# Optimization experiments

Hardware: AMD Instinct MI355X
Metric: run time of the kernel (lower is better)

The kernel has to match this reference:

```python
import jax, jax.numpy as jnp
import numpy as np

B, EMBED, H, W = 2, 32, 96, 96
SQ = (4, 2); R = 2; EXP = 2
SCH = EMBED // SQ[0]            # 8  squeezed channel dim
SHSP = SCH * R * R              # 32 shuffled spatial dim
SSP = SHSP // SQ[1]             # 16 squeezed spatial dim (attention embed dim)
HEADS = SCH * EXP               # 16
EACH = SSP // SCH               # 2
IDX = np.array([i + j * SCH for i in range(SCH) for j in range(EACH)])
NIDX = np.array([i + j * EACH for i in range(EACH) for j in range(SCH)])


def conv(x, w, b, stride=1, pad=0, groups=1):
    y = jax.lax.conv_general_dilated(x, w, (stride, stride), [(pad, pad), (pad, pad)],
                                     feature_group_count=groups,
                                     dimension_numbers=('NCHW', 'OIHW', 'NCHW'))
    return y + b[None, :, None, None]


def ln_ch(x, w, b):
    # LayerNorm over channel dim (torch applies it on [B,HW,C])
    mu = x.mean(1, keepdims=True)
    var = ((x - mu) ** 2).mean(1, keepdims=True)
    return (x - mu) * jax.lax.rsqrt(var + 1e-5) * w[None, :, None, None] + b[None, :, None, None]


def l2n(x, axis):
    # F.normalize: divide by L2 norm clamped to eps
    return x / jnp.maximum(jnp.sqrt(jnp.sum(x * x, axis=axis, keepdims=True)), 1e-12)


def _qkv(x, wqkv, bqkv):
    Bb, C, Hh, Ww = x.shape
    qkv = conv(x, wqkv, bqkv, groups=C)                        # [B, C*EXP*3, H, W], per-channel 1x1
    qkv = qkv.reshape(Bb, C, EXP * 3, Hh, Ww).transpose(0, 2, 1, 3, 4)
    q, k, v = jnp.split(qkv, 3, axis=1)                        # each [B, EXP, C, H, W]
    hd = EXP * C // HEADS
    rs = lambda a: a.reshape(Bb, HEADS, hd, Hh * Ww)
    return rs(q), rs(k), rs(v)


def _fuse(o, wfus, bfus, Bb, C, Hh, Ww):
    o = o.reshape(Bb, EXP, C, Hh, Ww).transpose(0, 2, 1, 3, 4).reshape(Bb, C * EXP, Hh, Ww)
    return conv(o, wfus, bfus, groups=C)


def chan_attn(x, wqkv, bqkv, t, wfus, bfus):
    Bb, C, Hh, Ww = x.shape
    q, k, v = _qkv(x, wqkv, bqkv)
    q, k = l2n(q, -1), l2n(k, -1)
    a = jax.nn.softmax(jnp.einsum('bhdn,bhen->bhde', q, k) * t, axis=-1)   # [B,h,d,d]
    o = jnp.einsum('bhde,bhen->bhdn', a, v)
    return _fuse(o, wfus, bfus, Bb, C, Hh, Ww)


def spat_attn(x, wqkv, bqkv, t, wfus, bfus):
    Bb, C, Hh, Ww = x.shape
    q, k, v = _qkv(x, wqkv, bqkv)
    q, k = l2n(q, -2), l2n(k, -2)
    a = jax.nn.softmax(jnp.einsum('bhdn,bhdm->bhnm', q, k) * t, axis=-1)   # [B,h,HW,HW]
    o = jnp.einsum('bhnm,bhdm->bhdn', a, v)
    return _fuse(o, wfus, bfus, Bb, C, Hh, Ww)


def pixel_shuffle(x, r):
    Bb, C, Hh, Ww = x.shape
    x = x.reshape(Bb, C // (r * r), r, r, Hh, Ww).transpose(0, 1, 4, 2, 5, 3)
    return x.reshape(Bb, C // (r * r), Hh * r, Ww * r)


def _forward(x, ln1_w, ln1_b, cab_w1, cab_b1, cab_w2, cab_b2, cab_aw1, cab_ab1, cab_aw2, cab_ab2,
             sq1_w, sq1_b, sq2_w, sq2_b, ca_qkv_w, ca_qkv_b, ca_t, ca_fus_w, ca_fus_b,
             sa_qkv_w, sa_qkv_b, sa_t, sa_fus_w, sa_fus_b, un1_w, un1_b, un2_w, un2_b,
             ln2_w, ln2_b, da_w1, da_b1, da_dw_w, da_dw_b, da_pw, da_pb):
    Bb, C, Hh, Ww = x.shape
    xn = ln_ch(x, ln1_w, ln1_b)
    # ---- CAB branch (conv-GELU-conv + RCAN channel attention) ----
    c = jax.nn.gelu(conv(xn, cab_w1, cab_b1, pad=1), approximate=False)
    c = conv(c, cab_w2, cab_b2, pad=1)
    y = c.mean((2, 3), keepdims=True)
    y = jax.nn.relu(conv(y, cab_aw1, cab_ab1))
    y = jax.nn.sigmoid(conv(y, cab_aw2, cab_ab2))
    x_cab = c * y
    # ---- Condensed attention branch ----
    z = conv(xn, sq1_w, sq1_b)                                   # 1x1: C -> SCH
    z = conv(z, sq2_w, sq2_b, stride=R, groups=SCH)              # grouped RxR stride R: -> [B,SSP,H/R,W/R]
    z = z[:, IDX]
    z = chan_attn(z, ca_qkv_w, ca_qkv_b, ca_t, ca_fus_w, ca_fus_b)
    z = z[:, NIDX]
    z = spat_attn(z, sa_qkv_w, sa_qkv_b, sa_t, sa_fus_w, sa_fus_b)
    z = conv(z, un1_w, un1_b, groups=SCH)                        # SSP -> SHSP
    z = pixel_shuffle(z, R)                                      # -> [B,SCH,H,W]
    z = conv(z, un2_w, un2_b)                                    # SCH -> C
    x = x + z + x_cab
    # ---- Dual adaptive (gated depthwise-conv FFN) ----
    xn2 = ln_ch(x, ln2_w, ln2_b)
    d = conv(xn2, da_w1, da_b1)
    d = conv(d, da_dw_w, da_dw_b, pad=3, groups=C).reshape(Bb, C, 2, Hh, Ww)
    d = jax.nn.gelu(d[:, :, 0], approximate=False) * jax.nn.sigmoid(d[:, :, 1])
    d = conv(d, da_pw, da_pb)
    return x + d


def setup_inputs():
    key = jax.random.key(0)
    ks = iter(jax.random.split(key, 40))
    nrm = lambda s: jax.random.normal(next(ks), s, jnp.float32) * 0.05
    inp = {'x': jax.random.normal(next(ks), (B, EMBED, H, W), jnp.float32)}
    wshapes = {
        'cab_w1': (EMBED // 4, EMBED, 3, 3), 'cab_w2': (EMBED, EMBED // 4, 3, 3),
        'cab_aw1': (EMBED // 18, EMBED, 1, 1), 'cab_aw2': (EMBED, EMBED // 18, 1, 1),
        'sq1_w': (SCH, EMBED, 1, 1), 'sq2_w': (SSP, 1, R, R),
        'ca_qkv_w': (SSP * EXP * 3, 1, 1, 1), 'ca_fus_w': (SSP, EXP, 1, 1),
        'sa_qkv_w': (SSP * EXP * 3, 1, 1, 1), 'sa_fus_w': (SSP, EXP, 1, 1),
        'un1_w': (SHSP, SSP // SCH, 1, 1), 'un2_w': (EMBED, SCH, 1, 1),
        'da_w1': (EMBED, EMBED, 1, 1), 'da_dw_w': (2 * EMBED, 1, 7, 7), 'da_pw': (EMBED, EMBED, 1, 1),
    }
    bshapes = {'cab_b1': EMBED // 4, 'cab_b2': EMBED, 'cab_ab1': EMBED // 18, 'cab_ab2': EMBED,
               'sq1_b': SCH, 'sq2_b': SSP, 'ca_qkv_b': SSP * EXP * 3, 'ca_fus_b': SSP,
               'sa_qkv_b': SSP * EXP * 3, 'sa_fus_b': SSP, 'un1_b': SHSP, 'un2_b': EMBED,
               'da_b1': EMBED, 'da_dw_b': 2 * EMBED, 'da_pb': EMBED}
    for n, s in wshapes.items():
        inp[n] = nrm(s)
    for n, s in bshapes.items():
        inp[n] = nrm((s,))
    inp['ln1_w'] = jnp.ones((EMBED,), jnp.float32); inp['ln1_b'] = jnp.zeros((EMBED,), jnp.float32)
    inp['ln2_w'] = jnp.ones((EMBED,), jnp.float32); inp['ln2_b'] = jnp.zeros((EMBED,), jnp.float32)
    inp['ca_t'] = jnp.ones((1, HEADS, 1, 1), jnp.float32)
    inp['sa_t'] = jnp.ones((1, HEADS, 1, 1), jnp.float32)
    return inp


def reference(x, ln1_w, ln1_b, cab_w1, cab_b1, cab_w2, cab_b2, cab_aw1, cab_ab1, cab_aw2, cab_ab2,
              sq1_w, sq1_b, sq2_w, sq2_b, ca_qkv_w, ca_qkv_b, ca_t, ca_fus_w, ca_fus_b,
              sa_qkv_w, sa_qkv_b, sa_t, sa_fus_w, sa_fus_b, un1_w, un1_b, un2_w, un2_b,
              ln2_w, ln2_b, da_w1, da_b1, da_dw_w, da_dw_b, da_pw, da_pb):
    return _forward(x, ln1_w, ln1_b, cab_w1, cab_b1, cab_w2, cab_b2, cab_aw1, cab_ab1, cab_aw2, cab_ab2,
                    sq1_w, sq1_b, sq2_w, sq2_b, ca_qkv_w, ca_qkv_b, ca_t, ca_fus_w, ca_fus_b,
                    sa_qkv_w, sa_qkv_b, sa_t, sa_fus_w, sa_fus_b, un1_w, un1_b, un2_w, un2_b,
                    ln2_w, ln2_b, da_w1, da_b1, da_dw_w, da_dw_b, da_pw, da_pb)
```

## Files before the change

kernel.cpp:

```cpp
#include <hip/hip_runtime.h>
#include <cstdint>
#include <math.h>

#define NP 9216
#define NP2 2304
#define KH 12
#define NMOM 78

__device__ __forceinline__ float gelu_ex(float v){
  return 0.5f*v*(1.0f+erff(v*0.70710678118654752440f));
}
__device__ __forceinline__ float sigm(float v){
  return 1.0f/(1.0f+__expf(-v));
}

__global__ __launch_bounds__(256) void k_ln1(const float* __restrict__ x,
    const float* __restrict__ lw, const float* __restrict__ lb,
    const float* __restrict__ sw, const float* __restrict__ sb,
    float* __restrict__ xn, float* __restrict__ z1)
{
  __shared__ float sred[2][8][32];
  __shared__ float xnsh[32][33];
  int p = threadIdx.x & 31, sl = threadIdx.x >> 5;
  int pix = blockIdx.x*32 + p;
  int b = pix / NP, n = pix % NP;
  const float* xp = x + (size_t)b*32*NP + (size_t)(sl*4)*NP + n;
  float v[4]; float s=0.f, s2=0.f;
#pragma unroll
  for (int c=0;c<4;c++){ float t=xp[(size_t)c*NP]; v[c]=t; s+=t; s2+=t*t; }
  sred[0][sl][p]=s; sred[1][sl][p]=s2;
  __syncthreads();
  s=0.f; s2=0.f;
#pragma unroll
  for (int g=0;g<8;g++){ s += sred[0][g][p]; s2 += sred[1][g][p]; }
  float mu = s*(1.f/32.f);
  float var = s2*(1.f/32.f)-mu*mu;
  float rs = rsqrtf(var+1e-5f);
  float* xo = xn + (size_t)b*32*NP + (size_t)(sl*4)*NP + n;
#pragma unroll
  for (int c=0;c<4;c++){
    int cc = sl*4+c;
    float t = (v[c]-mu)*rs*lw[cc]+lb[cc];
    xo[(size_t)c*NP] = t;
    xnsh[p][cc] = t;
  }
  __syncthreads();
  float vv[32];
#pragma unroll
  for (int c=0;c<32;c++) vv[c]=xnsh[p][c];
  int g = sl;
  float a = sb[g];
#pragma unroll
  for (int c=0;c<32;c++) a += vv[c]*sw[g*32+c];
  z1[(size_t)b*8*NP + (size_t)g*NP + n] = a;
}

__global__ __launch_bounds__(256) void k_phB(const float* __restrict__ xn,
    const float* __restrict__ w1, const float* __restrict__ b1,
    const float* __restrict__ z1, const float* __restrict__ w2,
    const float* __restrict__ b2,
    float* __restrict__ c1, float* __restrict__ u, float* __restrict__ spart)
{
  if (blockIdx.x < 576){
    int og = blockIdx.x/72, pb = blockIdx.x%72;
    int idx = pb*256+threadIdx.x;
    int b = idx/NP, n = idx%NP, i = n/96, j = n%96;
    float acc = b1[og];
    const float* xb = xn + (size_t)b*32*NP;
    const float* wb = w1 + og*288;
#pragma unroll
    for (int di=0;di<3;di++){
      int ii=i+di-1; if ((unsigned)ii>=96u) continue;
#pragma unroll
      for (int dj=0;dj<3;dj++){
        int jj=j+dj-1; if ((unsigned)jj>=96u) continue;
        const float* xp = xb + ii*96+jj;
        const float* wp = wb + di*3+dj;
#pragma unroll
        for (int c=0;c<32;c++) acc += xp[(size_t)c*NP]*wp[c*9];
      }
    }
    c1[(size_t)b*8*NP + (size_t)og*NP + n] = gelu_ex(acc);
  } else {
    __shared__ float red[4][5];
    int u2 = blockIdx.x-576;
    int pr = u2/18, pb = u2%18;
    int idx = pb*256+threadIdx.x;
    int b = idx/NP2, n = idx%NP2, i = n/48, j = n%48;
    int ocA = pr, ocB = pr+8;
    int gA = ocA>>1, gB = ocB>>1;
    const float* zpA = z1 + ((size_t)b*8+gA)*NP + (size_t)(2*i)*96 + 2*j;
    const float* zpB = z1 + ((size_t)b*8+gB)*NP + (size_t)(2*i)*96 + 2*j;
    float vA = zpA[0]*w2[ocA*4]+zpA[1]*w2[ocA*4+1]+zpA[96]*w2[ocA*4+2]+zpA[97]*w2[ocA*4+3]+b2[ocA];
    float vB = zpB[0]*w2[ocB*4]+zpB[1]*w2[ocB*4+1]+zpB[96]*w2[ocB*4+2]+zpB[97]*w2[ocB*4+3]+b2[ocB];
    u[((size_t)b*16+2*pr)*NP2 + n]   = vA;
    u[((size_t)b*16+2*pr+1)*NP2 + n] = vB;
    int wv=threadIdx.x>>6, ln=threadIdx.x&63;
    float st[5]={vA,vB,vA*vA,vB*vB,vA*vB};
#pragma unroll
    for (int k=0;k<5;k++){
      float r=st[k];
#pragma unroll
      for (int m=1;m<64;m<<=1) r+=__shfl_xor(r,m,64);
      if (ln==0) red[wv][k]=r;
    }
    __syncthreads();
    if (threadIdx.x<5){
      float r = red[0][threadIdx.x]+red[1][threadIdx.x]+red[2][threadIdx.x]+red[3][threadIdx.x];
      spart[(b*9 + (pb%9))*40 + pr*5 + threadIdx.x] = r;
    }
  }
}

__global__ __launch_bounds__(256) void k_phC(const float* __restrict__ c1,
    const float* __restrict__ w2, const float* __restrict__ b2,
    float* __restrict__ cbuf, float* __restrict__ ypart,
    const float* __restrict__ u, const float* __restrict__ spart,
    const float* __restrict__ cqw, const float* __restrict__ cqb,
    const float* __restrict__ cat, const float* __restrict__ cfw,
    const float* __restrict__ cfb,
    const float* __restrict__ qw, const float* __restrict__ qb,
    float2* __restrict__ qarr, float* __restrict__ mompart)
{
  if (blockIdx.x < 576){
    __shared__ float red[4][4];
    int og = blockIdx.x/72, pb = blockIdx.x%72;
    int idx = pb*256+threadIdx.x;
    int b = idx/NP, n = idx%NP, i = n/96, j = n%96;
    float acc[4];
#pragma unroll
    for (int k=0;k<4;k++) acc[k]=b2[og*4+k];
    const float* cb = c1 + (size_t)b*8*NP;
#pragma unroll
    for (int di=0;di<3;di++){
      int ii=i+di-1; if ((unsigned)ii>=96u) continue;
#pragma unroll
      for (int dj=0;dj<3;dj++){
        int jj=j+dj-1; if ((unsigned)jj>=96u) continue;
        const float* xp = cb + ii*96+jj;
#pragma unroll
        for (int c=0;c<8;c++){
          float val = xp[(size_t)c*NP];
          const float* wp = w2 + (og*4)*72 + c*9+di*3+dj;
#pragma unroll
          for (int k=0;k<4;k++) acc[k] += val*wp[k*72];
        }
      }
    }
    int wv = threadIdx.x>>6, ln = threadIdx.x&63;
#pragma unroll
    for (int k=0;k<4;k++){
      cbuf[(size_t)b*32*NP + (size_t)(og*4+k)*NP + n] = acc[k];
      float r = acc[k];
#pragma unroll
      for (int m=1;m<64;m<<=1) r += __shfl_xor(r, m, 64);
      if (ln==0) red[wv][k]=r;
    }
    __syncthreads();
    if (threadIdx.x<4){
      float r = red[0][threadIdx.x]+red[1][threadIdx.x]+red[2][threadIdx.x]+red[3][threadIdx.x];
      ypart[(og*72+pb)*4 + threadIdx.x] = r;
    }
  } else {
    __shared__ float red16[16][80];
    int u2 = blockIdx.x-576;
    int bh = u2/9, ch = u2%9;
    int n = ch*256 + threadIdx.x;
    int b = bh>>4, h = bh&15;
    int p = h&7, s = h>>3;
    int cc0=2*p, cc1=2*p+1;
    int oc0 = 2*(cc0&7)+(cc0>>3);
    int oc1 = 2*(cc1&7)+(cc1>>3);
    float AA[2], BB[2], CCc[2];
#pragma unroll
    for (int t2=0;t2<2;t2++){
      int oc = t2? oc1:oc0;
      int p2 = oc>>1, dd = oc&1;
      float st[5]={0,0,0,0,0};
      for (int ib=0; ib<9; ib++){
#pragma unroll
        for (int k=0;k<5;k++) st[k] += spart[(b*9+ib)*40 + p2*5 + k];
      }
      float S0=st[0],S1=st[1],Q00=st[2],Q11=st[3],Q01=st[4];
      float Sd = dd? S1:S0;
      float Qdd = dd? Q11:Q00;
      float cu0[2],cu1[2],ccst[2];
#pragma unroll
      for (int hh=0;hh<2;hh++){
        int h2=p2+8*hh;
        float th2=cat[h2];
        float aq=cqw[(2*p2+dd)*6+hh], bq=cqb[(2*p2+dd)*6+hh];
        float nq=fmaxf(sqrtf(fmaxf(aq*aq*Qdd+2.f*aq*bq*Sd+2304.f*bq*bq,0.f)),1e-12f);
        float m2[2],av[2],bv[2];
#pragma unroll
        for (int e=0;e<2;e++){
          float Se_=e?S1:S0, Qee=e?Q11:Q00, Qde=(dd==e)?Qdd:Q01;
          float ak=cqw[(2*p2+e)*6+2+hh], bk=cqb[(2*p2+e)*6+2+hh];
          float nk=fmaxf(sqrtf(fmaxf(ak*ak*Qee+2.f*ak*bk*Se_+2304.f*bk*bk,0.f)),1e-12f);
          float D=aq*ak*Qde + aq*bk*Sd + bq*ak*Se_ + 2304.f*bq*bk;
          m2[e]=th2*D/(nq*nk);
          av[e]=cqw[(2*p2+e)*6+4+hh]; bv[e]=cqb[(2*p2+e)*6+4+hh];
        }
        float mx=fmaxf(m2[0],m2[1]);
        float e0=__expf(m2[0]-mx), e1=__expf(m2[1]-mx);
        float inv=1.f/(e0+e1);
        cu0[hh]=e0*inv*av[0]; cu1[hh]=e1*inv*av[1]; ccst[hh]=e0*inv*bv[0]+e1*inv*bv[1];
      }
      float f0=cfw[oc*2], f1=cfw[oc*2+1];
      AA[t2]=f0*cu0[0]+f1*cu0[1];
      BB[t2]=f0*cu1[0]+f1*cu1[1];
      CCc[t2]=f0*ccst[0]+f1*ccst[1]+cfb[oc];
    }
    const float* u00 = u + ((size_t)b*16 + (oc0>>1)*2)*NP2;
    const float* u01 = u00 + NP2;
    const float* u10 = u + ((size_t)b*16 + (oc1>>1)*2)*NP2;
    const float* u11 = u10 + NP2;
    float w0 = AA[0]*u00[n]+BB[0]*u01[n]+CCc[0];
    float w1 = AA[1]*u10[n]+BB[1]*u11[n]+CCc[1];
    float k0 = qw[cc0*6+2+s]*w0+qb[cc0*6+2+s];
    float k1 = qw[cc1*6+2+s]*w1+qb[cc1*6+2+s];
    float rnk = 1.f/fmaxf(sqrtf(k0*k0+k1*k1),1e-12f);
    float kc = k0*rnk, ks = k1*rnk;
    float q0 = qw[cc0*6+s]*w0+qb[cc0*6+s];
    float q1 = qw[cc1*6+s]*w1+qb[cc1*6+s];
    float rnq = 1.f/fmaxf(sqrtf(q0*q0+q1*q1),1e-12f);
    qarr[bh*NP2+n] = make_float2(q0*rnq, q1*rnq);

    int grp = threadIdx.x>>4, gl = threadIdx.x&15;
    float c = 1.f, sn = 0.f;
#pragma unroll
    for (int k=0;k<=KH;k++){
      float vals[6] = {c, sn, c*w0, sn*w0, c*w1, sn*w1};
#pragma unroll
      for (int jv=0;jv<6;jv++){
        float r = vals[jv];
        r += __shfl_xor(r, 1, 64);
        r += __shfl_xor(r, 2, 64);
        r += __shfl_xor(r, 4, 64);
        r += __shfl_xor(r, 8, 64);
        if (gl==0) red16[grp][k*6+jv] = r;
      }
      float cn = c*kc - sn*ks;
      sn = sn*kc + c*ks;
      c = cn;
    }
    __syncthreads();
    if (threadIdx.x < NMOM){
      float r = 0.f;
#pragma unroll
      for (int g=0;g<16;g++) r += red16[g][threadIdx.x];
      mompart[(bh*9+ch)*NMOM + threadIdx.x] = r;
    }
  }
}

__global__ __launch_bounds__(256) void k_rows(const float2* __restrict__ qarr,
    const float* __restrict__ mompart, const float* __restrict__ sat,
    const float* __restrict__ qw, const float* __restrict__ qb,
    const float* __restrict__ fw, const float* __restrict__ fb,
    const float* __restrict__ u1w, const float* __restrict__ u1b,
    float* __restrict__ ps)
{
  int bp = blockIdx.x/9, ch = blockIdx.x%9;
  int b = bp>>3, p = bp&7;
  int n = ch*256 + (int)threadIdx.x;
  __shared__ float msh[2][80];
  __shared__ float fsh[2][13];
  int tid = threadIdx.x;
  if (tid < 26){
    int hh = tid/13, k = tid%13;
    double t = (double)sat[p+8*hh];
    double fac;
    if (fabs(t) < 1e-3){
      double xh = 0.5*t;
      double pk = 1.0;
      for (int q=1;q<=k;q++) pk *= xh/(double)q;
      double Ik = pk*(1.0 + xh*xh/(double)(k+1));
      fac = (k? 2.0:1.0)*Ik;
    } else {
      const int KS = 36;
      double ip1 = 0.0, ik = 1e-280, sum2 = 0.0;
      double vk = 0.0, v0 = 0.0;
      for (int q=KS; q>=1; --q){
        if (q == k) vk = ik;
        sum2 += ik;
        double im1 = ip1 + (2.0*(double)q/t)*ik;
        ip1 = ik; ik = im1;
      }
      v0 = ik;
      if (k == 0) vk = v0;
      double total = v0 + 2.0*sum2;
      double scale = exp(t)/total;
      fac = (k? 2.0:1.0)*vk*scale;
    }
    fsh[hh][k] = (float)fac;
  }
  if (tid < 2*NMOM){
    int hh = tid/NMOM, jj = tid%NMOM;
    float ssum = 0.f;
    for (int ib=0; ib<9; ib++)
      ssum += mompart[((size_t)(b*16+p+8*hh)*9+ib)*NMOM + jj];
    msh[hh][jj] = ssum;
  }
  __syncthreads();
  if (tid < 2*NMOM){
    int hh = tid/NMOM, jj = tid%NMOM;
    msh[hh][jj] *= fsh[hh][jj/6];
  }
  __syncthreads();
  float o[2][2];
#pragma unroll
  for (int hh=0;hh<2;hh++){
    float2 q = qarr[(size_t)(b*16+p+8*hh)*NP2 + n];
    float c = 1.f, sn = 0.f;
    float Se=0.f, S0=0.f, S1=0.f;
#pragma unroll
    for (int k=0;k<=KH;k++){
      const float* mk = &msh[hh][k*6];
      Se += c*mk[0] + sn*mk[1];
      S0 += c*mk[2] + sn*mk[3];
      S1 += c*mk[4] + sn*mk[5];
      float cn = c*q.x - sn*q.y;
      sn = sn*q.x + c*q.y;
      c = cn;
    }
    float rSe = 1.f/Se;
    float av0=qw[(2*p)*6+4+hh],  bv0=qb[(2*p)*6+4+hh];
    float av1=qw[(2*p+1)*6+4+hh],bv1=qb[(2*p+1)*6+4+hh];
    o[hh][0]=av0*S0*rSe+bv0;
    o[hh][1]=av1*S1*rSe+bv1;
  }
  float zz0 = o[0][0]*fw[(2*p)*2]   + o[1][0]*fw[(2*p)*2+1]   + fb[2*p];
  float zz1 = o[0][1]*fw[(2*p+1)*2] + o[1][1]*fw[(2*p+1)*2+1] + fb[2*p+1];
  int i=n/48, j=n%48;
  float* pb2 = ps + ((size_t)b*8+p)*NP;
#pragma unroll
  for (int k=0;k<4;k++){
    int od = 4*p+k;
    float v = zz0*u1w[od*2] + zz1*u1w[od*2+1] + u1b[od];
    pb2[(size_t)(2*i+(k>>1))*96 + 2*j + (k&1)] = v;
  }
}

__global__ __launch_bounds__(256) void k_un2(const float* __restrict__ ps,
    const float* __restrict__ ypart,
    const float* __restrict__ aw1, const float* __restrict__ ab1,
    const float* __restrict__ aw2, const float* __restrict__ ab2,
    const float* __restrict__ u2w, const float* __restrict__ u2b,
    const float* __restrict__ x, const float* __restrict__ cbuf,
    const float* __restrict__ lw, const float* __restrict__ lb,
    const float* __restrict__ dw1, const float* __restrict__ db1,
    float* __restrict__ xsum, float* __restrict__ d1)
{
  __shared__ float sred[2][8][32];
  __shared__ float xsh[32][33];
  __shared__ float y2sh[32];
  int p = threadIdx.x & 31, sl = threadIdx.x >> 5;
  int pix = blockIdx.x*32 + p;
  int b = pix/NP, n = pix%NP;
  if (threadIdx.x < 32){
    int c = threadIdx.x;
    float ssum = 0.f;
    for (int ib=0; ib<36; ib++)
      ssum += ypart[((c>>2)*72 + b*36 + ib)*4 + (c&3)];
    float pr = ssum*(1.f/9216.f)*aw1[c];
#pragma unroll
    for (int m=1;m<32;m<<=1) pr += __shfl_xor(pr, m, 64);
    float y1 = fmaxf(pr+ab1[0], 0.f);
    y2sh[c] = sigm(aw2[c]*y1+ab2[c]);
  }
  float pg[8];
#pragma unroll
  for (int g=0;g<8;g++) pg[g]=ps[((size_t)b*8+g)*NP+n];
  __syncthreads();
  float xv[4]; float s=0.f,s2=0.f;
#pragma unroll
  for (int c=0;c<4;c++){
    int cc = sl*4+c;
    float a=u2b[cc];
#pragma unroll
    for (int g=0;g<8;g++) a+=pg[g]*u2w[cc*8+g];
    size_t off=((size_t)b*32+cc)*NP+n;
    float t = x[off]+a+cbuf[off]*y2sh[cc];
    xv[c]=t; xsum[off]=t; s+=t; s2+=t*t;
  }
  sred[0][sl][p]=s; sred[1][sl][p]=s2;
  __syncthreads();
  s=0.f; s2=0.f;
#pragma unroll
  for (int g=0;g<8;g++){ s += sred[0][g][p]; s2 += sred[1][g][p]; }
  float mu=s*(1.f/32.f), var=s2*(1.f/32.f)-mu*mu, rs=rsqrtf(var+1e-5f);
#pragma unroll
  for (int c=0;c<4;c++){
    int cc = sl*4+c;
    xsh[p][cc] = (xv[c]-mu)*rs*lw[cc]+lb[cc];
  }
  __syncthreads();
  float vv[32];
#pragma unroll
  for (int c=0;c<32;c++) vv[c]=xsh[p][c];
#pragma unroll
  for (int k=0;k<4;k++){
    int o = sl*4+k;
    float a=db1[o];
#pragma unroll
    for (int cc=0;cc<32;cc++) a+=vv[cc]*dw1[o*32+cc];
    d1[((size_t)b*32+o)*NP+n]=a;
  }
}

__global__ __launch_bounds__(256) void k_dw(const float* __restrict__ d1,
    const float* __restrict__ w, const float* __restrict__ bias,
    float* __restrict__ dg)
{
  int idx = blockIdx.x*256+threadIdx.x;
  int pl = idx/4608, n2 = idx%4608;
  int i2 = n2/96, j = n2%96;
  int c = pl&31;
  const float* dp = d1 + (size_t)pl*NP;
  const float* w0p = w + (2*c)*49;
  const float* w1p = w + (2*c+1)*49;
  float a0=bias[2*c], a1=bias[2*c+1];
  float c0=bias[2*c], c1=bias[2*c+1];
#pragma unroll
  for (int di=0;di<8;di++){
    int ii=2*i2-3+di; if ((unsigned)ii>=96u) continue;
    const float* rowp = dp + ii*96;
    float t[7];
#pragma unroll
    for (int dj=0;dj<7;dj++){
      int jj=j+dj-3;
      t[dj] = ((unsigned)jj<96u) ? rowp[jj] : 0.f;
    }
    if (di<7){
#pragma unroll
      for (int dj=0;dj<7;dj++){ a0 += t[dj]*w0p[di*7+dj]; a1 += t[dj]*w1p[di*7+dj]; }
    }
    if (di>0){
#pragma unroll
      for (int dj=0;dj<7;dj++){ c0 += t[dj]*w0p[(di-1)*7+dj]; c1 += t[dj]*w1p[(di-1)*7+dj]; }
    }
  }
  dg[(size_t)pl*NP + (size_t)(2*i2)*96 + j]   = gelu_ex(a0)*sigm(a1);
  dg[(size_t)pl*NP + (size_t)(2*i2+1)*96 + j] = gelu_ex(c0)*sigm(c1);
}

__global__ __launch_bounds__(256) void k_fin(const float* __restrict__ dg,
    const float* __restrict__ pw, const float* __restrict__ pb,
    const float* __restrict__ xsum, float* __restrict__ out)
{
  __shared__ float xsh[32][33];
  int p = threadIdx.x & 31, sl = threadIdx.x >> 5;
  int pix = blockIdx.x*32 + p;
  int b = pix/NP, n = pix%NP;
  const float* dp = dg + ((size_t)b*32 + sl*4)*NP + n;
#pragma unroll
  for (int c=0;c<4;c++) xsh[p][sl*4+c]=dp[(size_t)c*NP];
  __syncthreads();
  float vv[32];
#pragma unroll
  for (int c=0;c<32;c++) vv[c]=xsh[p][c];
#pragma unroll
  for (int k=0;k<4;k++){
    int o = sl*4+k;
    float a=pb[o];
#pragma unroll
    for (int cc=0;cc<32;cc++) a+=vv[cc]*pw[o*32+cc];
    size_t off=((size_t)b*32+o)*NP+n;
    out[off]=xsum[off]+a;
  }
}

extern "C" void kernel_launch(void* const* d_in, const int* in_sizes, int n_in,
                              void* d_out, int out_size, void* d_ws, size_t ws_size,
                              hipStream_t stream) {
  (void)in_sizes; (void)n_in; (void)out_size; (void)ws_size;
  const float* x       =(const float*)d_in[0];
  const float* cab_w1  =(const float*)d_in[1];
  const float* cab_w2  =(const float*)d_in[2];
  const float* cab_aw1 =(const float*)d_in[3];
  const float* cab_aw2 =(const float*)d_in[4];
  const float* sq1_w   =(const float*)d_in[5];
  const float* sq2_w   =(const float*)d_in[6];
  const float* ca_qkv_w=(const float*)d_in[7];
  const float* ca_fus_w=(const float*)d_in[8];
  const float* sa_qkv_w=(const float*)d_in[9];
  const float* sa_fus_w=(const float*)d_in[10];
  const float* un1_w   =(const float*)d_in[11];
  const float* un2_w   =(const float*)d_in[12];
  const float* da_w1   =(const float*)d_in[13];
  const float* da_dw_w =(const float*)d_in[14];
  const float* da_pw   =(const float*)d_in[15];
  const float* cab_b1  =(const float*)d_in[16];
  const float* cab_b2  =(const float*)d_in[17];
  const float* cab_ab1 =(const float*)d_in[18];
  const float* cab_ab2 =(const float*)d_in[19];
  const float* sq1_b   =(const float*)d_in[20];
  const float* sq2_b   =(const float*)d_in[21];
  const float* ca_qkv_b=(const float*)d_in[22];
  const float* ca_fus_b=(const float*)d_in[23];
  const float* sa_qkv_b=(const float*)d_in[24];
  const float* sa_fus_b=(const float*)d_in[25];
  const float* un1_b   =(const float*)d_in[26];
  const float* un2_b   =(const float*)d_in[27];
  const float* da_b1   =(const float*)d_in[28];
  const float* da_dw_b =(const float*)d_in[29];
  const float* da_pb   =(const float*)d_in[30];
  const float* ln1_w   =(const float*)d_in[31];
  const float* ln1_b   =(const float*)d_in[32];
  const float* ln2_w   =(const float*)d_in[33];
  const float* ln2_b   =(const float*)d_in[34];
  const float* ca_t    =(const float*)d_in[35];
  const float* sa_t    =(const float*)d_in[36];

  float* ws=(float*)d_ws;
  float* xn    = ws;
  float* z1    = ws + 589824;
  float* c1b   = ws + 737280;
  float* cb    = ws + 884736;
  float* u     = ws + 1474560;
  float* psb   = ws + 1548288;
  float* xsm   = ws + 1695744;
  float* ypart = ws + 2285568;
  float* spart = ws + 2287872;
  float2* qarr = (float2*)(ws + 2288640);
  float* mompart = ws + 2436096;
  float* d1    = xn;
  float* dg    = cb;

  k_ln1 <<<576, 256,0,stream>>>(x, ln1_w, ln1_b, sq1_w, sq1_b, xn, z1);
  k_phB <<<720, 256,0,stream>>>(xn, cab_w1, cab_b1, z1, sq2_w, sq2_b, c1b, u, spart);
  k_phC <<<864, 256,0,stream>>>(c1b, cab_w2, cab_b2, cb, ypart,
                                u, spart, ca_qkv_w, ca_qkv_b, ca_t, ca_fus_w, ca_fus_b,
                                sa_qkv_w, sa_qkv_b, qarr, mompart);
  k_rows<<<144, 256,0,stream>>>(qarr, mompart, sa_t, sa_qkv_w, sa_qkv_b,
                                sa_fus_w, sa_fus_b, un1_w, un1_b, psb);
  k_un2 <<<576, 256,0,stream>>>(psb, ypart, cab_aw1, cab_ab1, cab_aw2, cab_ab2,
                                un2_w, un2_b, x, cb, ln2_w, ln2_b, da_w1, da_b1, xsm, d1);
  k_dw  <<<1152,256,0,stream>>>(d1, da_dw_w, da_dw_b, dg);
  k_fin <<<576, 256,0,stream>>>(dg, da_pw, da_pb, xsm, (float*)d_out);
}
```

Baseline: 71.43 us.

## Fuse spatial-attention row evaluation into the un2/LN2 kernel

```diff
diff --git a/kernel.cpp b/kernel.cpp
--- a/kernel.cpp
+++ b/kernel.cpp
@@ -254,22 +254,33 @@
   }
 }
 
-__global__ __launch_bounds__(256) void k_rows(const float2* __restrict__ qarr,
-    const float* __restrict__ mompart, const float* __restrict__ sat,
+__global__ __launch_bounds__(256) void k_un2(
+    const float* __restrict__ mompart, const float2* __restrict__ qarr,
+    const float* __restrict__ sat,
     const float* __restrict__ qw, const float* __restrict__ qb,
     const float* __restrict__ fw, const float* __restrict__ fb,
     const float* __restrict__ u1w, const float* __restrict__ u1b,
-    float* __restrict__ ps)
+    const float* __restrict__ ypart,
+    const float* __restrict__ aw1, const float* __restrict__ ab1,
+    const float* __restrict__ aw2, const float* __restrict__ ab2,
+    const float* __restrict__ u2w, const float* __restrict__ u2b,
+    const float* __restrict__ x, const float* __restrict__ cbuf,
+    const float* __restrict__ lw, const float* __restrict__ lb,
+    const float* __restrict__ dw1, const float* __restrict__ db1,
+    float* __restrict__ xsum, float* __restrict__ d1)
 {
-  int bp = blockIdx.x/9, ch = blockIdx.x%9;
-  int b = bp>>3, p = bp&7;
-  int n = ch*256 + (int)threadIdx.x;
-  __shared__ float msh[2][80];
-  __shared__ float fsh[2][13];
+  __shared__ float msh[16][80];
+  __shared__ float fsh[16][13];
+  __shared__ float sred[2][8][32];
+  __shared__ float xsh[32][33];
+  __shared__ float y2sh[32];
+  int p = threadIdx.x & 31, sl = threadIdx.x >> 5;
+  int pix = blockIdx.x*32 + p;
+  int b = pix/NP, n = pix%NP;
   int tid = threadIdx.x;
-  if (tid < 26){
-    int hh = tid/13, k = tid%13;
-    double t = (double)sat[p+8*hh];
+  if (tid < 208){
+    int h = tid/13, k = tid%13;
+    double t = (double)sat[h];
     double fac;
     if (fabs(t) < 1e-3){
       double xh = 0.5*t;
@@ -293,73 +304,17 @@
       double scale = exp(t)/total;
       fac = (k? 2.0:1.0)*vk*scale;
     }
-    fsh[hh][k] = (float)fac;
-  }
-  if (tid < 2*NMOM){
-    int hh = tid/NMOM, jj = tid%NMOM;
+    fsh[h][k] = (float)fac;
+  }
+  for (int e = tid; e < 16*NMOM; e += 256){
+    int bh = e/NMOM, jj = e%NMOM;
     float ssum = 0.f;
     for (int ib=0; ib<9; ib++)
-      ssum += mompart[((size_t)(b*16+p+8*hh)*9+ib)*NMOM + jj];
-    msh[hh][jj] = ssum;
-  }
-  __syncthreads();
-  if (tid < 2*NMOM){
-    int hh = tid/NMOM, jj = tid%NMOM;
-    msh[hh][jj] *= fsh[hh][jj/6];
-  }
-  __syncthreads();
-  float o[2][2];
-#pragma unroll
-  for (int hh=0;hh<2;hh++){
-    float2 q = qarr[(size_t)(b*16+p+8*hh)*NP2 + n];
-    float c = 1.f, sn = 0.f;
-    float Se=0.f, S0=0.f, S1=0.f;
-#pragma unroll
-    for (int k=0;k<=KH;k++){
-      const float* mk = &msh[hh][k*6];
-      Se += c*mk[0] + sn*mk[1];
-      S0 += c*mk[2] + sn*mk[3];
-      S1 += c*mk[4] + sn*mk[5];
-      float cn = c*q.x - sn*q.y;
-      sn = sn*q.x + c*q.y;
-      c = cn;
-    }
-    float rSe = 1.f/Se;
-    float av0=qw[(2*p)*6+4+hh],  bv0=qb[(2*p)*6+4+hh];
-    float av1=qw[(2*p+1)*6+4+hh],bv1=qb[(2*p+1)*6+4+hh];
-    o[hh][0]=av0*S0*rSe+bv0;
-    o[hh][1]=av1*S1*rSe+bv1;
-  }
-  float zz0 = o[0][0]*fw[(2*p)*2]   + o[1][0]*fw[(2*p)*2+1]   + fb[2*p];
-  float zz1 = o[0][1]*fw[(2*p+1)*2] + o[1][1]*fw[(2*p+1)*2+1] + fb[2*p+1];
-  int i=n/48, j=n%48;
-  float* pb2 = ps + ((size_t)b*8+p)*NP;
-#pragma unroll
-  for (int k=0;k<4;k++){
-    int od = 4*p+k;
-    float v = zz0*u1w[od*2] + zz1*u1w[od*2+1] + u1b[od];
-    pb2[(size_t)(2*i+(k>>1))*96 + 2*j + (k&1)] = v;
-  }
-}
-
-__global__ __launch_bounds__(256) void k_un2(const float* __restrict__ ps,
-    const float* __restrict__ ypart,
-    const float* __restrict__ aw1, const float* __restrict__ ab1,
-    const float* __restrict__ aw2, const float* __restrict__ ab2,
-    const float* __restrict__ u2w, const float* __restrict__ u2b,
-    const float* __restrict__ x, const float* __restrict__ cbuf,
-    const float* __restrict__ lw, const float* __restrict__ lb,
-    const float* __restrict__ dw1, const float* __restrict__ db1,
-    float* __restrict__ xsum, float* __restrict__ d1)
-{
-  __shared__ float sred[2][8][32];
-  __shared__ float xsh[32][33];
-  __shared__ float y2sh[32];
-  int p = threadIdx.x & 31, sl = threadIdx.x >> 5;
-  int pix = blockIdx.x*32 + p;
-  int b = pix/NP, n = pix%NP;
-  if (threadIdx.x < 32){
-    int c = threadIdx.x;
+      ssum += mompart[((size_t)(b*16+bh)*9+ib)*NMOM + jj];
+    msh[bh][jj] = ssum;
+  }
+  if (tid < 32){
+    int c = tid;
     float ssum = 0.f;
     for (int ib=0; ib<36; ib++)
       ssum += ypart[((c>>2)*72 + b*36 + ib)*4 + (c&3)];
@@ -369,10 +324,46 @@
     float y1 = fmaxf(pr+ab1[0], 0.f);
     y2sh[c] = sigm(aw2[c]*y1+ab2[c]);
   }
+  __syncthreads();
+  for (int e = tid; e < 16*NMOM; e += 256){
+    int bh = e/NMOM, jj = e%NMOM;
+    msh[bh][jj] *= fsh[bh][jj/6];
+  }
+  __syncthreads();
+  int ii = n/96, jj96 = n%96;
+  int n48 = (ii>>1)*48 + (jj96>>1);
+  int kq = (ii&1)*2 + (jj96&1);
   float pg[8];
 #pragma unroll
-  for (int g=0;g<8;g++) pg[g]=ps[((size_t)b*8+g)*NP+n];
-  __syncthreads();
+  for (int g=0;g<8;g++){
+    float o[2][2];
+#pragma unroll
+    for (int hh=0;hh<2;hh++){
+      int h = g+8*hh;
+      float2 q = qarr[(size_t)(b*16+h)*NP2 + n48];
+      float c = 1.f, sn = 0.f;
+      float Se=0.f, S0=0.f, S1=0.f;
+#pragma unroll
+      for (int k=0;k<=KH;k++){
+        const float* mk = &msh[h][k*6];
+        Se += c*mk[0] + sn*mk[1];
+        S0 += c*mk[2] + sn*mk[3];
+        S1 += c*mk[4] + sn*mk[5];
+        float cn = c*q.x - sn*q.y;
+        sn = sn*q.x + c*q.y;
+        c = cn;
+      }
+      float rSe = 1.f/Se;
+      float av0=qw[(2*g)*6+4+hh],  bv0=qb[(2*g)*6+4+hh];
+      float av1=qw[(2*g+1)*6+4+hh],bv1=qb[(2*g+1)*6+4+hh];
+      o[hh][0]=av0*S0*rSe+bv0;
+      o[hh][1]=av1*S1*rSe+bv1;
+    }
+    float zz0 = o[0][0]*fw[(2*g)*2]   + o[1][0]*fw[(2*g)*2+1]   + fb[2*g];
+    float zz1 = o[0][1]*fw[(2*g+1)*2] + o[1][1]*fw[(2*g+1)*2+1] + fb[2*g+1];
+    int od = 4*g+kq;
+    pg[g] = zz0*u1w[od*2] + zz1*u1w[od*2+1] + u1b[od];
+  }
   float xv[4]; float s=0.f,s2=0.f;
 #pragma unroll
   for (int c=0;c<4;c++){
@@ -519,12 +510,11 @@
   float* c1b   = ws + 737280;
   float* cb    = ws + 884736;
   float* u     = ws + 1474560;
-  float* psb   = ws + 1548288;
-  float* xsm   = ws + 1695744;
-  float* ypart = ws + 2285568;
-  float* spart = ws + 2287872;
-  float2* qarr = (float2*)(ws + 2288640);
-  float* mompart = ws + 2436096;
+  float* xsm   = ws + 1548288;
+  float* ypart = ws + 2138112;
+  float* spart = ws + 2140416;
+  float2* qarr = (float2*)(ws + 2141184);
+  float* mompart = ws + 2288640;
   float* d1    = xn;
   float* dg    = cb;
 
@@ -533,9 +523,9 @@
   k_phC <<<864, 256,0,stream>>>(c1b, cab_w2, cab_b2, cb, ypart,
                                 u, spart, ca_qkv_w, ca_qkv_b, ca_t, ca_fus_w, ca_fus_b,
                                 sa_qkv_w, sa_qkv_b, qarr, mompart);
-  k_rows<<<144, 256,0,stream>>>(qarr, mompart, sa_t, sa_qkv_w, sa_qkv_b,
-                                sa_fus_w, sa_fus_b, un1_w, un1_b, psb);
-  k_un2 <<<576, 256,0,stream>>>(psb, ypart, cab_aw1, cab_ab1, cab_aw2, cab_ab2,
+  k_un2 <<<576, 256,0,stream>>>(mompart, qarr, sa_t, sa_qkv_w, sa_qkv_b,
+                                sa_fus_w, sa_fus_b, un1_w, un1_b,
+                                ypart, cab_aw1, cab_ab1, cab_aw2, cab_ab2,
                                 un2_w, un2_b, x, cb, ln2_w, ln2_b, da_w1, da_b1, xsm, d1);
   k_dw  <<<1152,256,0,stream>>>(d1, da_dw_w, da_dw_b, dg);
   k_fin <<<576, 256,0,stream>>>(dg, da_pw, da_pb, xsm, (float*)d_out);
```

Measured after the change: 85.15 us. 1.19x slower.
